# Kernel tuning notes

Hardware: AMD Instinct MI355X
Metric: run time of the kernel (lower is better)

## Reference

```python
import jax, jax.numpy as jnp
import numpy as np

B, C, H, W = 2, 128, 128, 128
K, STRIDE, DIL, NH = 8, 2, 2, 8
HID = int(C * 4 / 3)  # 170


def _ln(x, g, b):
    # layernorm2d: normalize over channel axis (last axis in NHWC)
    mu = jnp.mean(x, axis=-1, keepdims=True)
    xc = x - mu
    var = jnp.mean(xc * xc, axis=-1, keepdims=True)
    return xc * jax.lax.rsqrt(var + 1e-6) * g + b


def _nat_attn(xn, qkv_w, qkv_b, qg, qb, kg, kb, proj_w, proj_b):
    # dilated/strided local-neighborhood attention (NATTEN-style)
    Bq, Hq, Wq, Cq = xn.shape
    dh = Cq // NH
    qkv = xn @ qkv_w.T + qkv_b
    q, k, v = jnp.split(qkv, 3, axis=-1)
    q = _ln(q, qg, qb)
    k = _ln(k, kg, kb)
    # keys/values on a stride-subsampled grid
    kc = k[:, ::STRIDE, ::STRIDE, :]
    vc = v[:, ::STRIDE, ::STRIDE, :]
    Hc, Wc = Hq // STRIDE, Wq // STRIDE
    plo = DIL * (K // 2)
    phi = DIL * (K - 1 - K // 2)
    pad = ((0, 0), (plo, phi), (plo, phi), (0, 0))
    kp = jnp.pad(kc, pad)
    vp = jnp.pad(vc, pad)
    mp = jnp.pad(jnp.ones((1, Hc, Wc, 1), dtype=bool), pad)
    offs = [(i * DIL, j * DIL) for i in range(K) for j in range(K)]  # fixed k*k window taps
    kn = jnp.stack([kp[:, a:a + Hc, b:b + Wc, :] for a, b in offs], axis=3).reshape(Bq, Hc, Wc, K * K, NH, dh)
    vn = jnp.stack([vp[:, a:a + Hc, b:b + Wc, :] for a, b in offs], axis=3).reshape(Bq, Hc, Wc, K * K, NH, dh)
    mn = jnp.stack([mp[:, a:a + Hc, b:b + Wc, 0] for a, b in offs], axis=3)  # [1,Hc,Wc,kk]
    # each full-res query maps to its coarse kv cell: [B,Hc,stride,Wc,stride,heads,dh]
    q6 = q.reshape(Bq, Hc, STRIDE, Wc, STRIDE, NH, dh)
    scores = jnp.einsum('bisjtnd,bijknd->bisjtnk', q6, kn) * (dh ** -0.5)
    m = mn[:, :, None, :, None, None, :]
    scores = jnp.where(m, scores, jnp.float32(-1e30))
    attn = jax.nn.softmax(scores, axis=-1)
    out = jnp.einsum('bisjtnk,bijknd->bisjtnd', attn, vn).reshape(Bq, Hq, Wq, Cq)
    return out @ proj_w.T + proj_b


def _cffn(xn, fc1_w, fc1_b, mg, mb, fc2_w, fc2_b):
    h = xn @ fc1_w.T + fc1_b
    h = _ln(h, mg, mb)
    h = jax.nn.gelu(h, approximate=True)  # gelu_tanh
    return h @ fc2_w.T + fc2_b


def setup_inputs():
    key = jax.random.key(0)
    ks = jax.random.split(key, 6)
    w = lambda k, shp: jax.random.normal(k, shp, dtype=jnp.float32) * 0.02
    z = lambda n: jnp.zeros((n,), jnp.float32)
    o = lambda n: jnp.ones((n,), jnp.float32)
    return {
        'x': jax.random.normal(ks[0], (B, C, H, W), dtype=jnp.float32),
        'qkv_w': w(ks[1], (3 * C, C)), 'qkv_b': z(3 * C),
        'qg': o(C), 'qb': z(C), 'kg': o(C), 'kb': z(C),
        'proj_w': w(ks[2], (C, C)), 'proj_b': z(C),
        'n1g': o(C), 'n1b': z(C), 'n2g': o(C), 'n2b': z(C),
        'ls1_g': jnp.full((C,), 1e-5, jnp.float32),
        'ls2_g': jnp.full((C,), 1e-5, jnp.float32),
        'fc1_w': w(ks[3], (HID, C)), 'fc1_b': z(HID),
        'mg': o(HID), 'mb': z(HID),
        'fc2_w': w(ks[4], (C, HID)), 'fc2_b': z(C),
    }


def reference(x, qkv_w, qkv_b, qg, qb, kg, kb, proj_w, proj_b, n1g, n1b, n2g, n2b, ls1_g, ls2_g, fc1_w, fc1_b, mg, mb, fc2_w, fc2_b):
    xh = jnp.transpose(x, (0, 2, 3, 1))  # NCHW -> NHWC
    xh = xh + ls1_g * _nat_attn(_ln(xh, n1g, n1b), qkv_w, qkv_b, qg, qb, kg, kb, proj_w, proj_b)
    xh = xh + ls2_g * _cffn(_ln(xh, n2g, n2b), fc1_w, fc1_b, mg, mb, fc2_w, fc2_b)
    return jnp.transpose(xh, (0, 3, 1, 2))
```

## Files before the change

### kernel.cpp

```cpp
#include <hip/hip_runtime.h>
#include <hip/hip_bf16.h>

typedef __hip_bfloat16 BF;
typedef __attribute__((ext_vector_type(8))) short bf16x8;
typedef __attribute__((ext_vector_type(4))) float f32x4;
typedef __attribute__((ext_vector_type(4))) unsigned short us4;


#define ASTR 200
#define KSTR 136

__device__ __forceinline__ unsigned cvt2(float lo, float hi){
  unsigned r;
  asm("v_cvt_pk_bf16_f32 %0, %1, %2" : "=v"(r) : "v"(lo), "v"(hi));
  return r;
}
__device__ __forceinline__ bf16x8 pk8(float4 a, float4 b){
  union{ unsigned u[4]; bf16x8 v; } c;
  c.u[0] = cvt2(a.x, a.y); c.u[1] = cvt2(a.z, a.w);
  c.u[2] = cvt2(b.x, b.y); c.u[3] = cvt2(b.z, b.w);
  return c.v;
}

__device__ __forceinline__ void gsum16h(float v[16], float* red, int tid){
  #pragma unroll
  for(int s = 1; s < 64; s <<= 1){
    #pragma unroll
    for(int i = 0; i < 16; i++) v[i] += __shfl_xor(v[i], s);
  }
  const int wid = tid >> 6, half = tid >> 7;
  __syncthreads();
  if((tid & 63) == 0){
    #pragma unroll
    for(int i = 0; i < 16; i++) red[wid*16 + i] = v[i];
  }
  __syncthreads();
  #pragma unroll
  for(int i = 0; i < 16; i++) v[i] = red[half*32 + i] + red[half*32 + 16 + i];
}

__device__ __forceinline__ void rowredh(float s1[4], float s2[4], float* red, int tid){
  const int lane = tid & 63, wid = tid >> 6, half = tid >> 7;
  #pragma unroll
  for(int m = 1; m < 16; m <<= 1){
    #pragma unroll
    for(int r = 0; r < 4; r++){ s1[r] += __shfl_xor(s1[r], m); s2[r] += __shfl_xor(s2[r], m); }
  }
  const int q4 = lane >> 4;
  __syncthreads();
  if((lane & 15) == 0){
    #pragma unroll
    for(int r = 0; r < 4; r++){
      red[wid*32 + q4*4 + r]      = s1[r];
      red[wid*32 + 16 + q4*4 + r] = s2[r];
    }
  }
  __syncthreads();
  #pragma unroll
  for(int r = 0; r < 4; r++){
    s1[r] = red[half*64 + q4*4 + r]      + red[half*64 + 32 + q4*4 + r];
    s2[r] = red[half*64 + 16 + q4*4 + r] + red[half*64 + 48 + q4*4 + r];
  }
}

__device__ __forceinline__ void rowred4(float s1[4], float s2[4], float* red,
                                        int wave, int lane){
  #pragma unroll
  for(int m = 1; m < 16; m <<= 1){
    #pragma unroll
    for(int r = 0; r < 4; r++){ s1[r] += __shfl_xor(s1[r], m); s2[r] += __shfl_xor(s2[r], m); }
  }
  const int q4 = lane >> 4;
  __syncthreads();
  if((lane & 15) == 0){
    #pragma unroll
    for(int r = 0; r < 4; r++){
      red[wave*32 + q4*4 + r]      = s1[r];
      red[wave*32 + 16 + q4*4 + r] = s2[r];
    }
  }
  __syncthreads();
  #pragma unroll
  for(int r = 0; r < 4; r++){
    s1[r] = red[q4*4 + r] + red[32 + q4*4 + r] + red[64 + q4*4 + r] + red[96 + q4*4 + r];
    s2[r] = red[16 + q4*4 + r] + red[48 + q4*4 + r] + red[80 + q4*4 + r] + red[112 + q4*4 + r];
  }
}

__global__ void __launch_bounds__(256)
k_pre(const float* __restrict__ x,
      const float* __restrict__ qkv_w, const float* __restrict__ proj_w,
      const float* __restrict__ fc1_w, const float* __restrict__ fc2_w,
      const float* __restrict__ qkv_b,
      const float* __restrict__ kg, const float* __restrict__ kb,
      const float* __restrict__ n1g, const float* __restrict__ n1b,
      BF* __restrict__ pk,
      float* __restrict__ kcb, float* __restrict__ vcb){
  __shared__ __align__(16) unsigned char sm[9216];
  const int bx = blockIdx.x, tid = threadIdx.x;

  if(bx >= 512){
    const int idx = (bx - 512) * 256 + tid;
    if(idx >= 112640) return;
    float val;
    if(idx < 49152){
      const int reg = idx >> 14, l = idx & 16383;
      const int j = l & 7, q = (l>>3)&3, n = (l>>5)&127, s = l>>12;
      val = qkv_w[(reg*128 + n)*128 + (s*32 + q*8 + j)];
    } else if(idx < 65536){
      const int l = idx - 49152;
      const int j = l&7, q=(l>>3)&3, n=(l>>5)&127, s=l>>12;
      val = proj_w[n*128 + (s*32+q*8+j)];
    } else if(idx < 88064){
      const int l = idx - 65536;
      const int j = l&7, q=(l>>3)&3, rem = l>>5;
      const int n = rem % 176, s = rem / 176;
      const int k = s*32+q*8+j;
      val = (n < 170) ? fc1_w[n*128 + k] : 0.f;
    } else {
      const int l = idx - 88064;
      const int j = l&7, q=(l>>3)&3, n=(l>>5)&127, s=l>>12;
      const int k = s*32+q*8+j;
      val = (k < 170) ? fc2_w[n*170 + k] : 0.f;
    }
    pk[idx] = __float2bfloat16(val);
    return;
  }

  BF* const Abuf = (BF*)sm;
  float* const red = (float*)(sm + 8704);
  const int lane = tid & 63, half = tid >> 7, wh = (tid >> 6) & 1, c = tid & 127;
  const int l15 = lane & 15, q4 = lane >> 4;
  const int cp0 = bx * 16;
  const int b = cp0 >> 12, ic = (cp0 & 4095) >> 6, jb = cp0 & 63;
  BF* const AbufH = Abuf + half*16*KSTR;

  float xv[8];
  {
    const size_t off = (size_t)(b*128 + c)*16384 + (size_t)(2*ic)*128 + 2*(jb + half*8);
    const float4* xp4 = (const float4*)(x + off);
    const float4 f0 = xp4[0], f1 = xp4[1], f2 = xp4[2], f3 = xp4[3];
    xv[0]=f0.x; xv[1]=f0.z; xv[2]=f1.x; xv[3]=f1.z;
    xv[4]=f2.x; xv[5]=f2.z; xv[6]=f3.x; xv[7]=f3.z;
  }
  float st[16];
  #pragma unroll
  for(int r = 0; r < 8; r++){ st[r] = xv[r]; st[8+r] = xv[r]*xv[r]; }
  gsum16h(st, red, tid);
  {
    const float g = n1g[c], be = n1b[c];
    #pragma unroll
    for(int r = 0; r < 8; r++){
      const float mu = st[r]*(1.f/128.f);
      const float var = st[8+r]*(1.f/128.f) - mu*mu;
      AbufH[r*KSTR + c] = __float2bfloat16((xv[r]-mu)*rsqrtf(var+1e-6f)*g + be);
    }
  }
  __syncthreads();
  bf16x8 af[4];
  #pragma unroll
  for(int s = 0; s < 4; s++) af[s] = *(const bf16x8*)&AbufH[l15*KSTR + s*32 + q4*8];

  f32x4 acc[4];
  #pragma unroll
  for(int nt = 0; nt < 4; nt++){ acc[nt][0]=0.f; acc[nt][1]=0.f; acc[nt][2]=0.f; acc[nt][3]=0.f; }
  #pragma unroll
  for(int nt = 0; nt < 4; nt++){
    const int n = (wh*4+nt)*16 + l15;
    #pragma unroll
    for(int s = 0; s < 4; s++){
      const float* wp = qkv_w + (size_t)(128 + n)*128 + s*32 + q4*8;
      acc[nt] = __builtin_amdgcn_mfma_f32_16x16x32_bf16(
        af[s], pk8(*(const float4*)wp, *(const float4*)(wp+4)), acc[nt], 0,0,0);
    }
  }
  float s1[4], s2[4];
  #pragma unroll
  for(int r = 0; r < 4; r++){ s1[r]=0.f; s2[r]=0.f; }
  #pragma unroll
  for(int nt = 0; nt < 4; nt++){
    const float colb = qkv_b[128 + (wh*4+nt)*16 + l15];
    #pragma unroll
    for(int r = 0; r < 4; r++){
      const float vv = acc[nt][r] + colb;
      acc[nt][r] = vv; s1[r] += vv; s2[r] += vv*vv;
    }
  }
  rowredh(s1, s2, red, tid);
  #pragma unroll
  for(int nt = 0; nt < 4; nt++){
    const int col = (wh*4+nt)*16 + l15;
    const float g = kg[col], be = kb[col];
    #pragma unroll
    for(int r = 0; r < 4; r++){
      const int row = q4*4 + r;
      if(row < 8){
        const float mu = s1[r]*(1.f/128.f);
        const float var = s2[r]*(1.f/128.f) - mu*mu;
        kcb[(size_t)(cp0 + half*8 + row)*128 + col] = (acc[nt][r]-mu)*rsqrtf(var+1e-6f)*g + be;
      }
    }
  }
  #pragma unroll
  for(int nt = 0; nt < 4; nt++){ acc[nt][0]=0.f; acc[nt][1]=0.f; acc[nt][2]=0.f; acc[nt][3]=0.f; }
  #pragma unroll
  for(int nt = 0; nt < 4; nt++){
    const int n = (wh*4+nt)*16 + l15;
    #pragma unroll
    for(int s = 0; s < 4; s++){
      const float* wp = qkv_w + (size_t)(256 + n)*128 + s*32 + q4*8;
      acc[nt] = __builtin_amdgcn_mfma_f32_16x16x32_bf16(
        af[s], pk8(*(const float4*)wp, *(const float4*)(wp+4)), acc[nt], 0,0,0);
    }
  }
  #pragma unroll
  for(int nt = 0; nt < 4; nt++){
    const int col = (wh*4+nt)*16 + l15;
    const float bv = qkv_b[256 + col];
    #pragma unroll
    for(int r = 0; r < 4; r++){
      const int row = q4*4 + r;
      if(row < 8) vcb[(size_t)(cp0 + half*8 + row)*128 + col] = acc[nt][r] + bv;
    }
  }
}

__global__ void __launch_bounds__(256, 5)
k_cell(const float* __restrict__ x,
       const BF* __restrict__ packQ, const BF* __restrict__ packP,
       const BF* __restrict__ packF1, const BF* __restrict__ packF2,
       const float* __restrict__ qkv_b,
       const float* __restrict__ qg, const float* __restrict__ qb,
       const float* __restrict__ n1g, const float* __restrict__ n1b,
       const float* __restrict__ proj_b,
       const float* __restrict__ ls1, const float* __restrict__ ls2,
       const float* __restrict__ n2g, const float* __restrict__ n2b,
       const float* __restrict__ fc1_b,
       const float* __restrict__ mg, const float* __restrict__ mb,
       const float* __restrict__ fc2_b,
       const float* __restrict__ kcb, const float* __restrict__ vcb,
       float* __restrict__ out){
  __shared__ __align__(16) BF uni[9216];
  BF* const Abuf = uni;
  __shared__ float xvL[2048];
  __shared__ __align__(16) ushort qnH[2176];
  __shared__ ushort cidx2[256];
  float* const red = (float*)qnH;
  const int tid = threadIdx.x, wave = tid>>6, lane = tid&63;
  const int l15 = lane & 15, q4 = lane >> 4;

  const int bx0 = blockIdx.x;
  const int bx = ((bx0 & 7) << 8) | (bx0 >> 3);
  const int b = bx >> 10, rem = bx & 1023, ip = rem >> 5, jq = rem & 31;
  const int c = tid & 127, half = tid >> 7;

  float xv[8];
  {
    const size_t xb = (size_t)(b*128 + c)*16384 + (size_t)(4*ip + 2*half)*128 + 4*jq;
    const float4 r0 = *(const float4*)(x + xb);
    const float4 r1 = *(const float4*)(x + xb + 128);
    xv[0]=r0.x; xv[1]=r0.y; xv[2]=r0.z; xv[3]=r0.w;
    xv[4]=r1.x; xv[5]=r1.y; xv[6]=r1.z; xv[7]=r1.w;
    #pragma unroll
    for(int r = 0; r < 8; r++) xvL[(half*8 + r)*128 + c] = xv[r];
  }
  {
    const int cell = tid >> 6, e = tid & 63;
    const int i = e >> 3, j = e & 7;
    const int ic = 2*ip + (cell>>1), jcc = 2*jq + (cell&1);
    const int ri = ic + 2*i - 8, rj = jcc + 2*j - 8;
    const bool ok = (rj >= 0) && (rj < 64) && (ri >= 0) && (ri < 64);
    cidx2[cell*64 + e] = ok ? (ushort)(b*4096 + ri*64 + rj) : (ushort)0;
  }

  float st[16];
  #pragma unroll
  for(int r = 0; r < 8; r++){ st[r] = xv[r]; st[8+r] = xv[r]*xv[r]; }
  gsum16h(st, red, tid);
  {
    const float g = n1g[c], be = n1b[c];
    #pragma unroll
    for(int r = 0; r < 8; r++){
      const int p = half*8 + r;
      const float mu = st[r]*(1.f/128.f);
      const float var = st[8+r]*(1.f/128.f) - mu*mu;
      Abuf[p*ASTR + c] = __float2bfloat16((xv[r]-mu)*rsqrtf(var+1e-6f)*g + be);
    }
  }
  __syncthreads();

  {
    bf16x8 af[4];
    #pragma unroll
    for(int s = 0; s < 4; s++) af[s] = *(const bf16x8*)&Abuf[l15*ASTR + s*32 + q4*8];
    f32x4 acc[2];
    #pragma unroll
    for(int nt = 0; nt < 2; nt++){ acc[nt][0]=0.f; acc[nt][1]=0.f; acc[nt][2]=0.f; acc[nt][3]=0.f; }
    #pragma unroll
    for(int nt = 0; nt < 2; nt++){
      const int n = (wave*2+nt)*16 + l15;
      #pragma unroll
      for(int s = 0; s < 4; s++){
        bf16x8 bf = *(const bf16x8*)&packQ[((s*128 + n)*4 + q4)*8];
        acc[nt] = __builtin_amdgcn_mfma_f32_16x16x32_bf16(af[s], bf, acc[nt], 0,0,0);
      }
    }
    float s1[4], s2[4];
    #pragma unroll
    for(int r = 0; r < 4; r++){ s1[r]=0.f; s2[r]=0.f; }
    #pragma unroll
    for(int nt = 0; nt < 2; nt++){
      const float cb2 = qkv_b[(wave*2+nt)*16 + l15];
      #pragma unroll
      for(int r = 0; r < 4; r++){
        const float vv = acc[nt][r] + cb2;
        acc[nt][r] = vv; s1[r] += vv; s2[r] += vv*vv;
      }
    }
    rowred4(s1, s2, red, wave, lane);
    ushort tw[2][4];
    {
      float mu[4], rs[4];
      #pragma unroll
      for(int r = 0; r < 4; r++){
        mu[r] = s1[r]*(1.f/128.f);
        rs[r] = rsqrtf(s2[r]*(1.f/128.f) - mu[r]*mu[r] + 1e-6f);
      }
      #pragma unroll
      for(int nt = 0; nt < 2; nt++){
        const int col = (wave*2+nt)*16 + l15;
        const float g = qg[col], be = qb[col];
        float v0 = (acc[nt][0]-mu[0])*rs[0]*g + be;
        float v1 = (acc[nt][1]-mu[1])*rs[1]*g + be;
        float v2 = (acc[nt][2]-mu[2])*rs[2]*g + be;
        float v3 = (acc[nt][3]-mu[3])*rs[3]*g + be;
        const unsigned d0 = cvt2(v0, v1), d1 = cvt2(v2, v3);
        tw[nt][0] = (ushort)d0; tw[nt][1] = (ushort)(d0 >> 16);
        tw[nt][2] = (ushort)d1; tw[nt][3] = (ushort)(d1 >> 16);
      }
    }
    __syncthreads();
    #pragma unroll
    for(int nt = 0; nt < 2; nt++){
      const int col = (wave*2+nt)*16 + l15;
      const int colp = col + (col >> 4);
      #pragma unroll
      for(int r = 0; r < 4; r++){
        const int cell = 2*(q4>>1) + ((r>>1)&1);
        const int lp   = 2*(q4&1) + (r&1);
        qnH[cell*544 + colp*4 + lp] = tw[nt][r];
      }
    }
  }
  __syncthreads();

  const int hsub = l15 >> 2, px = l15 & 3;
  const int par = q4 >> 1, dbase = (q4 & 1) * 8;
  BF* const attw = uni + wave*2304;
  ushort* const Vt = (ushort*)attw;
  ushort* const Pb = (ushort*)(attw + 1152);
  const ushort* cidx = cidx2 + wave*64;
  const ushort* qp = qnH + wave*544;
  const int ic = 2*ip + (wave>>1), jcc = 2*jq + (wave&1);
  const int i0 = l15 >> 3;
  const int rj = jcc + 2*(l15 & 7) - 8;
  const bool vj = (rj >= 0) && (rj < 64);
  float madd[4];
  #pragma unroll
  for(int nt = 0; nt < 4; nt++){
    const int ri = ic + 2*(nt*2 + i0) - 8;
    madd[nt] = (vj && ri >= 0 && ri < 64) ? 0.f : -1e30f;
  }

  f32x4 oC[2];
  #pragma unroll
  for(int hg = 0; hg < 2; hg++){
    bf16x8 afq0, afq1;
    {
      const int idx0 = (hg*64 + hsub*16 + dbase + (hg*4 + hsub))*4 + px;
      short bq[8];
      #pragma unroll
      for(int j = 0; j < 8; j++) bq[j] = (short)qp[idx0 + 4*j];
      const bool a0 = (par == hsub), a1 = ((2 + par) == hsub);
      #pragma unroll
      for(int j = 0; j < 8; j++){
        afq0[j] = a0 ? bq[j] : (short)0;
        afq1[j] = a1 ? bq[j] : (short)0;
      }
    }
    f32x4 accq[4];
    #pragma unroll
    for(int nt = 0; nt < 4; nt++){ accq[nt][0]=0.f; accq[nt][1]=0.f; accq[nt][2]=0.f; accq[nt][3]=0.f; }
    #pragma unroll
    for(int nt = 0; nt < 4; nt++){
      const float* kp = kcb + ((size_t)cidx[nt*16 + l15] << 7) + hg*64 + q4*8;
      const float4 k00 = *(const float4*)kp;
      const float4 k01 = *(const float4*)(kp + 4);
      const float4 k10 = *(const float4*)(kp + 32);
      const float4 k11 = *(const float4*)(kp + 36);
      accq[nt] = __builtin_amdgcn_mfma_f32_16x16x32_bf16(afq0, pk8(k00,k01), accq[nt], 0,0,0);
      accq[nt] = __builtin_amdgcn_mfma_f32_16x16x32_bf16(afq1, pk8(k10,k11), accq[nt], 0,0,0);
    }
    float inv[4];
    #pragma unroll
    for(int reg = 0; reg < 4; reg++){
      const float s0 = accq[0][reg]*0.25f + madd[0];
      const float s1 = accq[1][reg]*0.25f + madd[1];
      const float s2 = accq[2][reg]*0.25f + madd[2];
      const float s3 = accq[3][reg]*0.25f + madd[3];
      float m = fmaxf(fmaxf(s0,s1), fmaxf(s2,s3));
      #pragma unroll
      for(int sft = 1; sft < 16; sft <<= 1) m = fmaxf(m, __shfl_xor(m, sft));
      const float e0 = __expf(s0-m), e1 = __expf(s1-m);
      const float e2 = __expf(s2-m), e3 = __expf(s3-m);
      ushort* pr = Pb + (q4*4 + reg)*72 + l15;
      const unsigned d0 = cvt2(e0, e1), d1 = cvt2(e2, e3);
      pr[0]  = (ushort)d0;
      pr[16] = (ushort)(d0 >> 16);
      pr[32] = (ushort)d1;
      pr[48] = (ushort)(d1 >> 16);
      float es = e0+e1+e2+e3;
      #pragma unroll
      for(int sft = 1; sft < 16; sft <<= 1) es += __shfl_xor(es, sft);
      inv[reg] = 1.f/es;
    }
    const bf16x8 pa0 = *(const bf16x8*)(Pb + l15*72 + q4*8);
    const bf16x8 pa1 = *(const bf16x8*)(Pb + l15*72 + 32 + q4*8);

    f32x4 oSel; oSel[0]=0.f; oSel[1]=0.f; oSel[2]=0.f; oSel[3]=0.f;
    #pragma unroll
    for(int hs = 0; hs < 4; hs++){
      const int h = hg*4 + hs;
      float4 vv[4];
      #pragma unroll
      for(int it = 0; it < 4; it++)
        vv[it] = *(const float4*)(vcb + ((size_t)cidx[l15*4 + it] << 7) + h*16 + q4*4);
      #pragma unroll
      for(int dd = 0; dd < 4; dd++){
        union{ unsigned u[2]; us4 v; } w;
        w.u[0] = cvt2(((const float*)&vv[0])[dd], ((const float*)&vv[1])[dd]);
        w.u[1] = cvt2(((const float*)&vv[2])[dd], ((const float*)&vv[3])[dd]);
        *(us4*)(Vt + (q4*4 + dd)*72 + l15*4) = w.v;
      }
      const bf16x8 bv0 = *(const bf16x8*)(Vt + l15*72 + q4*8);
      const bf16x8 bv1 = *(const bf16x8*)(Vt + l15*72 + 32 + q4*8);
      f32x4 accv; accv[0]=0.f; accv[1]=0.f; accv[2]=0.f; accv[3]=0.f;
      accv = __builtin_amdgcn_mfma_f32_16x16x32_bf16(pa0, bv0, accv, 0,0,0);
      accv = __builtin_amdgcn_mfma_f32_16x16x32_bf16(pa1, bv1, accv, 0,0,0);
      if(q4 == hs){ oSel[0]=accv[0]; oSel[1]=accv[1]; oSel[2]=accv[2]; oSel[3]=accv[3]; }
    }
    oC[hg][0] = oSel[0]*inv[0]; oC[hg][1] = oSel[1]*inv[1];
    oC[hg][2] = oSel[2]*inv[2]; oC[hg][3] = oSel[3]*inv[3];
  }
  __syncthreads();
  {
    ushort* ab = (ushort*)Abuf;
    #pragma unroll
    for(int hg = 0; hg < 2; hg++){
      const int col = (hg*4 + q4)*16 + l15;
      const unsigned d0 = cvt2(oC[hg][0], oC[hg][1]);
      const unsigned d1 = cvt2(oC[hg][2], oC[hg][3]);
      const ushort ov[4] = {(ushort)d0, (ushort)(d0>>16), (ushort)d1, (ushort)(d1>>16)};
      #pragma unroll
      for(int reg = 0; reg < 4; reg++){
        const int row_p = 8*(wave>>1) + 4*(reg>>1) + 2*(wave&1) + (reg&1);
        ab[row_p*ASTR + col] = ov[reg];
      }
    }
  }
  __syncthreads();

  float xh[2][4];
  {
    bf16x8 af[4];
    #pragma unroll
    for(int s = 0; s < 4; s++) af[s] = *(const bf16x8*)&Abuf[l15*ASTR + s*32 + q4*8];
    f32x4 acc[2];
    #pragma unroll
    for(int nt = 0; nt < 2; nt++){ acc[nt][0]=0.f; acc[nt][1]=0.f; acc[nt][2]=0.f; acc[nt][3]=0.f; }
    #pragma unroll
    for(int nt = 0; nt < 2; nt++){
      const int n = (wave*2+nt)*16 + l15;
      #pragma unroll
      for(int s = 0; s < 4; s++){
        bf16x8 bf = *(const bf16x8*)&packP[((s*128 + n)*4 + q4)*8];
        acc[nt] = __builtin_amdgcn_mfma_f32_16x16x32_bf16(af[s], bf, acc[nt], 0,0,0);
      }
    }
    float s1[4], s2[4];
    #pragma unroll
    for(int r = 0; r < 4; r++){ s1[r]=0.f; s2[r]=0.f; }
    #pragma unroll
    for(int nt = 0; nt < 2; nt++){
      const int col = (wave*2+nt)*16 + l15;
      const float bp = proj_b[col], l1 = ls1[col];
      #pragma unroll
      for(int r = 0; r < 4; r++){
        const int p = q4*4 + r;
        const float hx = xvL[p*128 + col] + l1*(acc[nt][r] + bp);
        xh[nt][r] = hx; s1[r] += hx; s2[r] += hx*hx;
      }
    }
    rowred4(s1, s2, red, wave, lane);
    #pragma unroll
    for(int nt = 0; nt < 2; nt++){
      const int col = (wave*2+nt)*16 + l15;
      const float g2 = n2g[col], be = n2b[col];
      #pragma unroll
      for(int r = 0; r < 4; r++){
        const int p = q4*4 + r;
        const float mu = s1[r]*(1.f/128.f);
        const float var = s2[r]*(1.f/128.f) - mu*mu;
        Abuf[p*ASTR + col] =
          __float2bfloat16((xh[nt][r]-mu)*rsqrtf(var+1e-6f)*g2 + be);
      }
    }
  }
  __syncthreads();

  {
    bf16x8 af[4];
    #pragma unroll
    for(int s = 0; s < 4; s++) af[s] = *(const bf16x8*)&Abuf[l15*ASTR + s*32 + q4*8];
    const int NT1 = (wave < 3) ? 3 : 2;
    const int tb  = (wave < 3) ? wave*3 : 9;
    f32x4 acc1[3];
    #pragma unroll
    for(int nt = 0; nt < 3; nt++){ acc1[nt][0]=0.f; acc1[nt][1]=0.f; acc1[nt][2]=0.f; acc1[nt][3]=0.f; }
    for(int nt = 0; nt < NT1; nt++){
      const int n = (tb + nt)*16 + l15;
      #pragma unroll
      for(int s = 0; s < 4; s++){
        bf16x8 bf = *(const bf16x8*)&packF1[((s*176 + n)*4 + q4)*8];
        acc1[nt] = __builtin_amdgcn_mfma_f32_16x16x32_bf16(af[s], bf, acc1[nt], 0,0,0);
      }
    }
    float s1[4], s2[4];
    #pragma unroll
    for(int r = 0; r < 4; r++){ s1[r]=0.f; s2[r]=0.f; }
    for(int nt = 0; nt < NT1; nt++){
      const int col = (tb + nt)*16 + l15;
      const float b1 = (col < 170) ? fc1_b[col] : 0.f;
      #pragma unroll
      for(int r = 0; r < 4; r++){
        const float vv = acc1[nt][r] + b1;
        acc1[nt][r] = vv; s1[r] += vv; s2[r] += vv*vv;
      }
    }
    rowred4(s1, s2, red, wave, lane);
    for(int z = tid; z < 352; z += 256){
      const int row = z / 22, colz = 170 + (z - (z/22)*22);
      Abuf[row*ASTR + colz] = __float2bfloat16(0.f);
    }
    const float kA = 0.7978845608028654f, kB = 0.044715f;
    for(int nt = 0; nt < NT1; nt++){
      const int col = (tb + nt)*16 + l15;
      if(col < 170){
        const float g2 = mg[col], be = mb[col];
        #pragma unroll
        for(int r = 0; r < 4; r++){
          const int p = q4*4 + r;
          const float mu = s1[r]*(1.f/170.f);
          const float var = s2[r]*(1.f/170.f) - mu*mu;
          const float hn = (acc1[nt][r]-mu)*rsqrtf(var+1e-6f)*g2 + be;
          const float u = kA*(hn + kB*hn*hn*hn);
          const float gl = hn / (1.f + __expf(-2.f*u));
          Abuf[p*ASTR + col] = __float2bfloat16(gl);
        }
      }
    }
  }
  __syncthreads();

  {
    bf16x8 af[6];
    #pragma unroll
    for(int s = 0; s < 6; s++) af[s] = *(const bf16x8*)&Abuf[l15*ASTR + s*32 + q4*8];
    f32x4 acc[2];
    #pragma unroll
    for(int nt = 0; nt < 2; nt++){ acc[nt][0]=0.f; acc[nt][1]=0.f; acc[nt][2]=0.f; acc[nt][3]=0.f; }
    #pragma unroll
    for(int nt = 0; nt < 2; nt++){
      const int n = (wave*2+nt)*16 + l15;
      #pragma unroll
      for(int s = 0; s < 6; s++){
        bf16x8 bf = *(const bf16x8*)&packF2[((s*128 + n)*4 + q4)*8];
        acc[nt] = __builtin_amdgcn_mfma_f32_16x16x32_bf16(af[s], bf, acc[nt], 0,0,0);
      }
    }
    #pragma unroll
    for(int nt = 0; nt < 2; nt++){
      const int col = (wave*2+nt)*16 + l15;
      const float bf2 = fc2_b[col], l2 = ls2[col];
      float4 o4;
      o4.x = xh[nt][0] + l2*(acc[nt][0] + bf2);
      o4.y = xh[nt][1] + l2*(acc[nt][1] + bf2);
      o4.z = xh[nt][2] + l2*(acc[nt][2] + bf2);
      o4.w = xh[nt][3] + l2*(acc[nt][3] + bf2);
      *(float4*)(out + (size_t)(b*128 + col)*16384 + (size_t)(4*ip + q4)*128 + 4*jq) = o4;
    }
  }
}

extern "C" void kernel_launch(void* const* d_in, const int* in_sizes, int n_in,
                              void* d_out, int out_size, void* d_ws, size_t ws_size,
                              hipStream_t stream){
  const float* x      = (const float*)d_in[0];
  const float* qkv_w  = (const float*)d_in[1];
  const float* qkv_b  = (const float*)d_in[2];
  const float* qg     = (const float*)d_in[3];
  const float* qb     = (const float*)d_in[4];
  const float* kg     = (const float*)d_in[5];
  const float* kb     = (const float*)d_in[6];
  const float* proj_w = (const float*)d_in[7];
  const float* proj_b = (const float*)d_in[8];
  const float* n1g    = (const float*)d_in[9];
  const float* n1b    = (const float*)d_in[10];
  const float* n2g    = (const float*)d_in[11];
  const float* n2b    = (const float*)d_in[12];
  const float* ls1    = (const float*)d_in[13];
  const float* ls2    = (const float*)d_in[14];
  const float* fc1_w  = (const float*)d_in[15];
  const float* fc1_b  = (const float*)d_in[16];
  const float* mg     = (const float*)d_in[17];
  const float* mb     = (const float*)d_in[18];
  const float* fc2_w  = (const float*)d_in[19];
  const float* fc2_b  = (const float*)d_in[20];

  float* ws  = (float*)d_ws;
  float* kcb = ws;
  float* vcb = ws + 1048576;
  BF* pk     = (BF*)(ws + 2097152);
  BF* packQ  = pk;
  BF* packP  = pk + 49152;
  BF* packF1 = pk + 65536;
  BF* packF2 = pk + 88064;

  k_pre <<<952, 256, 0, stream>>>(x, qkv_w, proj_w, fc1_w, fc2_w, qkv_b,
                                  kg, kb, n1g, n1b, pk, kcb, vcb);
  k_cell<<<2048, 256, 0, stream>>>(x, packQ, packP, packF1, packF2,
                                   qkv_b, qg, qb, n1g, n1b, proj_b, ls1, ls2,
                                   n2g, n2b, fc1_b, mg, mb, fc2_b,
                                   kcb, vcb, (float*)d_out);
}
```

Before: 230.9 us.

## Store V in padded column-parity layout and load MFMA operands directly

The value buffer is rewritten in k_pre into a zero-padded layout split by column parity, so each neighborhood row of strided taps sits in contiguous memory. k_cell then gathers the V operand for the PV MFMA straight from global memory into registers, with no LDS transpose through a Vt buffer. This halves the per-wave attention LDS scratch and raises the occupancy hint to 6. In exchange it adds a zeroing pass over the pad columns, a larger workspace, and more scattered scalar global loads per head.

```diff
diff --git a/kernel.cpp b/kernel.cpp
--- a/kernel.cpp
+++ b/kernel.cpp
@@ -4,7 +4,6 @@
 typedef __hip_bfloat16 BF;
 typedef __attribute__((ext_vector_type(8))) short bf16x8;
 typedef __attribute__((ext_vector_type(4))) float f32x4;
-typedef __attribute__((ext_vector_type(4))) unsigned short us4;
 
 
 #define ASTR 200
@@ -95,35 +94,43 @@
       const float* __restrict__ kg, const float* __restrict__ kb,
       const float* __restrict__ n1g, const float* __restrict__ n1b,
       BF* __restrict__ pk,
-      float* __restrict__ kcb, float* __restrict__ vcb){
+      float* __restrict__ kcb, float* __restrict__ vcbT){
   __shared__ __align__(16) unsigned char sm[9216];
   const int bx = blockIdx.x, tid = threadIdx.x;
 
   if(bx >= 512){
     const int idx = (bx - 512) * 256 + tid;
-    if(idx >= 112640) return;
-    float val;
-    if(idx < 49152){
-      const int reg = idx >> 14, l = idx & 16383;
-      const int j = l & 7, q = (l>>3)&3, n = (l>>5)&127, s = l>>12;
-      val = qkv_w[(reg*128 + n)*128 + (s*32 + q*8 + j)];
-    } else if(idx < 65536){
-      const int l = idx - 49152;
-      const int j = l&7, q=(l>>3)&3, n=(l>>5)&127, s=l>>12;
-      val = proj_w[n*128 + (s*32+q*8+j)];
-    } else if(idx < 88064){
-      const int l = idx - 65536;
-      const int j = l&7, q=(l>>3)&3, rem = l>>5;
-      const int n = rem % 176, s = rem / 176;
-      const int k = s*32+q*8+j;
-      val = (n < 170) ? fc1_w[n*128 + k] : 0.f;
-    } else {
-      const int l = idx - 88064;
-      const int j = l&7, q=(l>>3)&3, n=(l>>5)&127, s=l>>12;
-      const int k = s*32+q*8+j;
-      val = (k < 170) ? fc2_w[n*170 + k] : 0.f;
-    }
-    pk[idx] = __float2bfloat16(val);
+    if(idx < 112640){
+      float val;
+      if(idx < 49152){
+        const int reg = idx >> 14, l = idx & 16383;
+        const int j = l & 7, q = (l>>3)&3, n = (l>>5)&127, s = l>>12;
+        val = qkv_w[(reg*128 + n)*128 + (s*32 + q*8 + j)];
+      } else if(idx < 65536){
+        const int l = idx - 49152;
+        const int j = l&7, q=(l>>3)&3, n=(l>>5)&127, s=l>>12;
+        val = proj_w[n*128 + (s*32+q*8+j)];
+      } else if(idx < 88064){
+        const int l = idx - 65536;
+        const int j = l&7, q=(l>>3)&3, rem = l>>5;
+        const int n = rem % 176, s = rem / 176;
+        const int k = s*32+q*8+j;
+        val = (n < 170) ? fc1_w[n*128 + k] : 0.f;
+      } else {
+        const int l = idx - 88064;
+        const int j = l&7, q=(l>>3)&3, n=(l>>5)&127, s=l>>12;
+        const int k = s*32+q*8+j;
+        val = (k < 170) ? fc2_w[n*170 + k] : 0.f;
+      }
+      pk[idx] = __float2bfloat16(val);
+    }
+    for(int z = (bx - 512)*256 + tid; z < 262144; z += 440*256){
+      const int bpr = z >> 10;
+      const int pc  = (z >> 7) & 7;
+      const int d   = z & 127;
+      const int rjh5 = (pc < 5) ? pc : (32 + pc);
+      vcbT[((size_t)bpr*40 + rjh5)*128 + d] = 0.f;
+    }
     return;
   }
 
@@ -220,12 +227,18 @@
     #pragma unroll
     for(int r = 0; r < 4; r++){
       const int row = q4*4 + r;
-      if(row < 8) vcb[(size_t)(cp0 + half*8 + row)*128 + col] = acc[nt][r] + bv;
-    }
-  }
-}
-
-__global__ void __launch_bounds__(256, 5)
+      if(row < 8){
+        const int cp = cp0 + half*8 + row;
+        const int b2 = cp >> 12, rr = cp & 4095;
+        const int ri = rr >> 6, rj = rr & 63;
+        vcbT[((((size_t)(b2*2 + (rj&1))*64 + ri)*40) + (rj>>1) + 5)*128 + col]
+          = acc[nt][r] + bv;
+      }
+    }
+  }
+}
+
+__global__ void __launch_bounds__(256, 6)
 k_cell(const float* __restrict__ x,
        const BF* __restrict__ packQ, const BF* __restrict__ packP,
        const BF* __restrict__ packF1, const BF* __restrict__ packF2,
@@ -238,9 +251,9 @@
        const float* __restrict__ fc1_b,
        const float* __restrict__ mg, const float* __restrict__ mb,
        const float* __restrict__ fc2_b,
-       const float* __restrict__ kcb, const float* __restrict__ vcb,
+       const float* __restrict__ kcb, const float* __restrict__ vcbT,
        float* __restrict__ out){
-  __shared__ __align__(16) BF uni[9216];
+  __shared__ __align__(16) BF uni[4608];
   BF* const Abuf = uni;
   __shared__ float xvL[2048];
   __shared__ __align__(16) ushort qnH[2176];
@@ -355,10 +368,9 @@
   __syncthreads();
 
   const int hsub = l15 >> 2, px = l15 & 3;
-  const int par = q4 >> 1, dbase = (q4 & 1) * 8;
-  BF* const attw = uni + wave*2304;
-  ushort* const Vt = (ushort*)attw;
-  ushort* const Pb = (ushort*)(attw + 1152);
+  const int par4 = q4 >> 1, dbase = (q4 & 1) * 8;
+  BF* const attw = uni + wave*1152;
+  ushort* const Pb = (ushort*)attw;
   const ushort* cidx = cidx2 + wave*64;
   const ushort* qp = qnH + wave*544;
   const int ic = 2*ip + (wave>>1), jcc = 2*jq + (wave&1);
@@ -371,6 +383,11 @@
     const int ri = ic + 2*(nt*2 + i0) - 8;
     madd[nt] = (vj && ri >= 0 && ri < 64) ? 0.f : -1e30f;
   }
+  const int parv = jcc & 1;
+  const int riA = min(63, max(0, ic + 2*q4 - 8));
+  const int riB = min(63, max(0, ic + 2*q4));
+  const float* vbA = vcbT + ((((size_t)(b*2 + parv)*64 + riA)*40) + (jcc>>1) + 1)*128 + l15;
+  const float* vbB = vcbT + ((((size_t)(b*2 + parv)*64 + riB)*40) + (jcc>>1) + 1)*128 + l15;
 
   f32x4 oC[2];
   #pragma unroll
@@ -381,7 +398,7 @@
       short bq[8];
       #pragma unroll
       for(int j = 0; j < 8; j++) bq[j] = (short)qp[idx0 + 4*j];
-      const bool a0 = (par == hsub), a1 = ((2 + par) == hsub);
+      const bool a0 = (par4 == hsub), a1 = ((2 + par4) == hsub);
       #pragma unroll
       for(int j = 0; j < 8; j++){
         afq0[j] = a0 ? bq[j] : (short)0;
@@ -430,23 +447,21 @@
     f32x4 oSel; oSel[0]=0.f; oSel[1]=0.f; oSel[2]=0.f; oSel[3]=0.f;
     #pragma unroll
     for(int hs = 0; hs < 4; hs++){
-      const int h = hg*4 + hs;
-      float4 vv[4];
-      #pragma unroll
-      for(int it = 0; it < 4; it++)
-        vv[it] = *(const float4*)(vcb + ((size_t)cidx[l15*4 + it] << 7) + h*16 + q4*4);
-      #pragma unroll
-      for(int dd = 0; dd < 4; dd++){
-        union{ unsigned u[2]; us4 v; } w;
-        w.u[0] = cvt2(((const float*)&vv[0])[dd], ((const float*)&vv[1])[dd]);
-        w.u[1] = cvt2(((const float*)&vv[2])[dd], ((const float*)&vv[3])[dd]);
-        *(us4*)(Vt + (q4*4 + dd)*72 + l15*4) = w.v;
-      }
-      const bf16x8 bv0 = *(const bf16x8*)(Vt + l15*72 + q4*8);
-      const bf16x8 bv1 = *(const bf16x8*)(Vt + l15*72 + 32 + q4*8);
+      const int hoff = (hg*4 + hs)*16;
+      float a0[8], a1[8];
+      #pragma unroll
+      for(int j = 0; j < 8; j++){
+        a0[j] = vbA[j*128 + hoff];
+        a1[j] = vbB[j*128 + hoff];
+      }
+      union{ unsigned u[4]; bf16x8 v; } c0, c1;
+      c0.u[0]=cvt2(a0[0],a0[1]); c0.u[1]=cvt2(a0[2],a0[3]);
+      c0.u[2]=cvt2(a0[4],a0[5]); c0.u[3]=cvt2(a0[6],a0[7]);
+      c1.u[0]=cvt2(a1[0],a1[1]); c1.u[1]=cvt2(a1[2],a1[3]);
+      c1.u[2]=cvt2(a1[4],a1[5]); c1.u[3]=cvt2(a1[6],a1[7]);
       f32x4 accv; accv[0]=0.f; accv[1]=0.f; accv[2]=0.f; accv[3]=0.f;
-      accv = __builtin_amdgcn_mfma_f32_16x16x32_bf16(pa0, bv0, accv, 0,0,0);
-      accv = __builtin_amdgcn_mfma_f32_16x16x32_bf16(pa1, bv1, accv, 0,0,0);
+      accv = __builtin_amdgcn_mfma_f32_16x16x32_bf16(pa0, c0.v, accv, 0,0,0);
+      accv = __builtin_amdgcn_mfma_f32_16x16x32_bf16(pa1, c1.v, accv, 0,0,0);
       if(q4 == hs){ oSel[0]=accv[0]; oSel[1]=accv[1]; oSel[2]=accv[2]; oSel[3]=accv[3]; }
     }
     oC[hg][0] = oSel[0]*inv[0]; oC[hg][1] = oSel[1]*inv[1];
@@ -627,19 +642,19 @@
   const float* fc2_w  = (const float*)d_in[19];
   const float* fc2_b  = (const float*)d_in[20];
 
-  float* ws  = (float*)d_ws;
-  float* kcb = ws;
-  float* vcb = ws + 1048576;
-  BF* pk     = (BF*)(ws + 2097152);
-  BF* packQ  = pk;
-  BF* packP  = pk + 49152;
-  BF* packF1 = pk + 65536;
-  BF* packF2 = pk + 88064;
+  float* ws   = (float*)d_ws;
+  float* kcb  = ws;
+  float* vcbT = ws + 1048576;
+  BF* pk      = (BF*)(ws + 3670016);
+  BF* packQ   = pk;
+  BF* packP   = pk + 49152;
+  BF* packF1  = pk + 65536;
+  BF* packF2  = pk + 88064;
 
   k_pre <<<952, 256, 0, stream>>>(x, qkv_w, proj_w, fc1_w, fc2_w, qkv_b,
-                                  kg, kb, n1g, n1b, pk, kcb, vcb);
+                                  kg, kb, n1g, n1b, pk, kcb, vcbT);
   k_cell<<<2048, 256, 0, stream>>>(x, packQ, packP, packF1, packF2,
                                    qkv_b, qg, qb, n1g, n1b, proj_b, ls1, ls2,
                                    n2g, n2b, fc1_b, mg, mb, fc2_b,
-                                   kcb, vcb, (float*)d_out);
-}
+                                   kcb, vcbT, (float*)d_out);
+}
```

Measured after the change: 212.2 us. -8.1%, faster.
